# Kernel optimization log

Hardware: AMD Instinct MI355X
Metric: run time of the kernel (lower is better)

Reference implementation:

```python
import jax, jax.numpy as jnp
import numpy as np

# TT factorization of a 4096 -> 4096 linear layer
IN_SHAPE = (8, 8, 8, 8)    # input_tt_shape, prod = 4096
OUT_SHAPE = (8, 8, 8, 8)   # output_tt_shape, prod = 4096
RANKS = (1, 16, 16, 16, 1) # tt_ranks, len = n_dim + 1
N_DIM = len(IN_SHAPE)
BATCH = 2048
OUT_SIZE = int(np.prod(OUT_SHAPE))
IN_SIZE = int(np.prod(IN_SHAPE))


def setup_inputs() -> dict:
    key = jax.random.key(0)
    ks = jax.random.split(key, N_DIM + 1)
    x = jax.random.normal(ks[0], (BATCH, IN_SIZE), dtype=jnp.float32)
    inp = {"x": x}
    for i in range(N_DIM):
        rows = RANKS[i] * OUT_SHAPE[i]
        cols = IN_SHAPE[i] * RANKS[i + 1]
        # xavier_uniform scale, matching torch init statistics
        limit = float(np.sqrt(6.0 / (rows + cols)))
        inp[f"core{i}"] = jax.random.uniform(
            ks[i + 1], (rows, cols), minval=-limit, maxval=limit, dtype=jnp.float32
        )
    inp["bias"] = jnp.zeros((OUT_SIZE,), dtype=jnp.float32)
    return inp


def reference(x, core0, core1, core2, core3, bias):
    cores = [core0, core1, core2, core3]
    res = x  # [B, prod(IN_SHAPE)]
    # Sequential TT-core contraction, last mode first (faithful to torch loop)
    for k in range(N_DIM - 1, -1, -1):
        res = res.reshape(-1, IN_SHAPE[k])                     # [.., n_k]
        res = res.T                                            # [n_k, ..]
        res = res.reshape(RANKS[k + 1] * IN_SHAPE[k], -1)      # [r_{k+1}*n_k, ..]
        res = cores[k] @ res                                   # [r_k*m_k, ..]
    res = res.reshape(OUT_SIZE, -1).T                          # [B, prod(OUT_SHAPE)]
    return res + bias
```

## Files before the change

kernel.cpp:

```cpp
#include <hip/hip_runtime.h>
#include <hip/hip_bf16.h>
#include <stdint.h>


typedef __bf16 bf16_t;
typedef __bf16 bf16x8 __attribute__((ext_vector_type(8)));
typedef float floatx4 __attribute__((ext_vector_type(4)));

#define BATCH_N 2048
#define KD 4096
#define ND 4096

__device__ static inline void load_lds16(const void* g, void* l) {
    __builtin_amdgcn_global_load_lds(
        (const __attribute__((address_space(1))) void*)g,
        (__attribute__((address_space(3))) void*)l, 16, 0, 0);
}

__global__ __launch_bounds__(256) void cvt_x(const float* __restrict__ x,
                                             bf16_t* __restrict__ xb) {
    int t = blockIdx.x * 256 + threadIdx.x;
    const float4* xv = (const float4*)x;
    float4 a = xv[t * 2];
    float4 b = xv[t * 2 + 1];
    bf16x8 o;
    o[0] = (bf16_t)a.x; o[1] = (bf16_t)a.y; o[2] = (bf16_t)a.z; o[3] = (bf16_t)a.w;
    o[4] = (bf16_t)b.x; o[5] = (bf16_t)b.y; o[6] = (bf16_t)b.z; o[7] = (bf16_t)b.w;
    ((bf16x8*)xb)[t] = o;
}

__global__ __launch_bounds__(256) void build_w(const float* __restrict__ c0,
                                               const float* __restrict__ c1,
                                               const float* __restrict__ c2,
                                               const float* __restrict__ c3,
                                               bf16_t* __restrict__ W) {
    __shared__ float c0s[8 * 16];
    __shared__ float c1s[16 * 8 * 16];
    __shared__ float c2s[16 * 8 * 16];
    __shared__ float c3s[16 * 8];
    __shared__ float Ps[64 * 16];
    __shared__ float T1s[16 * 64];
    const int b = blockIdx.x;
    const int M23 = b >> 6, N01 = b & 63;
    const int n0 = N01 >> 3, n1 = N01 & 7, m2 = M23 >> 3, m3 = M23 & 7;
    const int t = threadIdx.x;

    if (t < 128) c0s[t] = c0[(t >> 4) * 128 + n0 * 16 + (t & 15)];
    if (t < 128) c3s[t] = c3[((t >> 3) * 8 + m3) * 8 + (t & 7)];
    for (int i = t; i < 2048; i += 256) {
        int r1 = i >> 7, m1 = (i >> 4) & 7, r2 = i & 15;
        c1s[i] = c1[(r1 * 8 + m1) * 128 + n1 * 16 + r2];
    }
    for (int i = t; i < 2048; i += 256) {
        int r2 = i >> 7, n2 = (i >> 4) & 7, r3 = i & 15;
        c2s[i] = c2[(r2 * 8 + m2) * 128 + n2 * 16 + r3];
    }
    __syncthreads();

    for (int i = t; i < 1024; i += 256) {
        int m01 = i >> 4, r2 = i & 15, m0 = m01 >> 3, m1 = m01 & 7;
        float s = 0.f;
#pragma unroll
        for (int r1 = 0; r1 < 16; ++r1)
            s += c0s[m0 * 16 + r1] * c1s[r1 * 128 + m1 * 16 + r2];
        Ps[i] = s;
    }
    for (int i = t; i < 1024; i += 256) {
        int r2 = i >> 6, n23 = i & 63, n2 = n23 >> 3, n3 = n23 & 7;
        float s = 0.f;
#pragma unroll
        for (int r3 = 0; r3 < 16; ++r3)
            s += c2s[r2 * 128 + n2 * 16 + r3] * c3s[r3 * 8 + n3];
        T1s[i] = s;
    }
    __syncthreads();

    const int n23 = t & 63, q = t >> 6;
#pragma unroll
    for (int g = 0; g < 16; ++g) {
        int m01 = q * 16 + g;
        float s = 0.f;
#pragma unroll
        for (int r2 = 0; r2 < 16; ++r2) s += Ps[m01 * 16 + r2] * T1s[r2 * 64 + n23];
        W[(size_t)(m01 * 64 + M23) * 4096 + N01 * 64 + n23] = (bf16_t)s;
    }
}

__global__ __launch_bounds__(256, 2) void gemm_bt(const bf16_t* __restrict__ A,
                                                  const bf16_t* __restrict__ B,
                                                  const float* __restrict__ bias,
                                                  float* __restrict__ C) {
    __shared__ bf16_t As[128 * 64];
    __shared__ bf16_t Bs[128 * 64];
    const int t = threadIdx.x;
    const int bn = blockIdx.x, bm = blockIdx.y;
    const int lane = t & 63, wave = t >> 6;
    const int wm = wave >> 1, wn = wave & 1;

    const int srow = lane >> 3;
    const int lc = (lane & 7) ^ srow;
    const bf16_t* Agp = A + (size_t)(bm * 128 + wave * 8 + srow) * KD + lc * 8;
    const bf16_t* Bgp = B + (size_t)(bn * 128 + wave * 8 + srow) * KD + lc * 8;
    bf16_t* AsW = As + wave * 512;
    bf16_t* BsW = Bs + wave * 512;

    floatx4 acc[4][4];
    floatx4 zero = {0.f, 0.f, 0.f, 0.f};
#pragma unroll
    for (int i = 0; i < 4; ++i)
#pragma unroll
        for (int j = 0; j < 4; ++j) acc[i][j] = zero;

    const int fr = lane & 15;
    const int fc = lane >> 4;

    for (int k0 = 0; k0 < KD; k0 += 64) {
        __syncthreads();
#pragma unroll
        for (int j = 0; j < 4; ++j) {
            load_lds16(Agp + (size_t)(j * 32) * KD + k0, AsW + j * 2048);
            load_lds16(Bgp + (size_t)(j * 32) * KD + k0, BsW + j * 2048);
        }
        __syncthreads();

#pragma unroll
        for (int kk = 0; kk < 2; ++kk) {
            const int pA = (fc + kk * 4) ^ (fr & 7);
            bf16x8 af[4], bf[4];
#pragma unroll
            for (int im = 0; im < 4; ++im)
                af[im] = *(const bf16x8*)(As + (wm * 64 + im * 16 + fr) * 64 + pA * 8);
#pragma unroll
            for (int in = 0; in < 4; ++in)
                bf[in] = *(const bf16x8*)(Bs + (wn * 64 + in * 16 + fr) * 64 + pA * 8);
#pragma unroll
            for (int im = 0; im < 4; ++im)
#pragma unroll
                for (int in = 0; in < 4; ++in)
                    acc[im][in] = __builtin_amdgcn_mfma_f32_16x16x32_bf16(
                        af[im], bf[in], acc[im][in], 0, 0, 0);
        }
    }

    const int rl = lane >> 4, cl = lane & 15;
    const size_t rbase = (size_t)bm * 128 + wm * 64;
    const int cbase = bn * 128 + wn * 64;
#pragma unroll
    for (int im = 0; im < 4; ++im) {
#pragma unroll
        for (int in = 0; in < 4; ++in) {
            int col = cbase + in * 16 + cl;
            float bv = bias[col];
#pragma unroll
            for (int r = 0; r < 4; ++r) {
                size_t row = rbase + im * 16 + rl * 4 + r;
                C[row * ND + col] = acc[im][in][r] + bv;
            }
        }
    }
}

extern "C" void kernel_launch(void* const* d_in, const int* in_sizes, int n_in,
                              void* d_out, int out_size, void* d_ws, size_t ws_size,
                              hipStream_t stream) {
    const float* x  = (const float*)d_in[0];
    const float* c0 = (const float*)d_in[1];
    const float* c1 = (const float*)d_in[2];
    const float* c2 = (const float*)d_in[3];
    const float* c3 = (const float*)d_in[4];
    const float* bias = (const float*)d_in[5];
    float* out = (float*)d_out;

    char* ws = (char*)d_ws;
    bf16_t* Xb = (bf16_t*)ws;
    bf16_t* W  = (bf16_t*)(ws + (16u << 20));

    cvt_x<<<4096, 256, 0, stream>>>(x, Xb);
    build_w<<<4096, 256, 0, stream>>>(c0, c1, c2, c3, W);
    dim3 grid(ND / 128, BATCH_N / 128);
    gemm_bt<<<grid, 256, 0, stream>>>(Xb, W, bias, out);
}
```

Measured before the change: 183.2 us.

## Replace LDS-tiled GEMM with register-direct loads and fuse prep kernels

The GEMM drops shared-memory staging and barriers. Each of two waves loads its A and B MFMA fragments straight from global memory into registers, double-buffered in 32-wide k steps, and each wave computes a 64x128 tile. The x conversion and W construction are merged into one launch to remove a kernel launch. The register path avoids LDS traffic and syncs but issues uncoalesced 16-byte row-strided global loads, gets no cross-wave reuse through LDS, and uses far more registers with fewer waves per block.

```diff
diff --git a/kernel.cpp b/kernel.cpp
--- a/kernel.cpp
+++ b/kernel.cpp
@@ -11,39 +11,36 @@
 #define KD 4096
 #define ND 4096
 
-__device__ static inline void load_lds16(const void* g, void* l) {
-    __builtin_amdgcn_global_load_lds(
-        (const __attribute__((address_space(1))) void*)g,
-        (__attribute__((address_space(3))) void*)l, 16, 0, 0);
-}
-
-__global__ __launch_bounds__(256) void cvt_x(const float* __restrict__ x,
-                                             bf16_t* __restrict__ xb) {
-    int t = blockIdx.x * 256 + threadIdx.x;
-    const float4* xv = (const float4*)x;
-    float4 a = xv[t * 2];
-    float4 b = xv[t * 2 + 1];
-    bf16x8 o;
-    o[0] = (bf16_t)a.x; o[1] = (bf16_t)a.y; o[2] = (bf16_t)a.z; o[3] = (bf16_t)a.w;
-    o[4] = (bf16_t)b.x; o[5] = (bf16_t)b.y; o[6] = (bf16_t)b.z; o[7] = (bf16_t)b.w;
-    ((bf16x8*)xb)[t] = o;
-}
-
-__global__ __launch_bounds__(256) void build_w(const float* __restrict__ c0,
-                                               const float* __restrict__ c1,
-                                               const float* __restrict__ c2,
-                                               const float* __restrict__ c3,
-                                               bf16_t* __restrict__ W) {
+__global__ __launch_bounds__(256) void prep(const float* __restrict__ x,
+                                            const float* __restrict__ c0,
+                                            const float* __restrict__ c1,
+                                            const float* __restrict__ c2,
+                                            const float* __restrict__ c3,
+                                            bf16_t* __restrict__ W,
+                                            bf16_t* __restrict__ xb) {
     __shared__ float c0s[8 * 16];
     __shared__ float c1s[16 * 8 * 16];
     __shared__ float c2s[16 * 8 * 16];
     __shared__ float c3s[16 * 8];
     __shared__ float Ps[64 * 16];
     __shared__ float T1s[16 * 64];
+    const int t = threadIdx.x;
+
+    if (blockIdx.x >= 4096) {
+        int g = (blockIdx.x - 4096) * 256 + t;
+        const float4* xv = (const float4*)x;
+        float4 a = xv[g * 2];
+        float4 b = xv[g * 2 + 1];
+        bf16x8 o;
+        o[0] = (bf16_t)a.x; o[1] = (bf16_t)a.y; o[2] = (bf16_t)a.z; o[3] = (bf16_t)a.w;
+        o[4] = (bf16_t)b.x; o[5] = (bf16_t)b.y; o[6] = (bf16_t)b.z; o[7] = (bf16_t)b.w;
+        ((bf16x8*)xb)[g] = o;
+        return;
+    }
+
     const int b = blockIdx.x;
     const int M23 = b >> 6, N01 = b & 63;
     const int n0 = N01 >> 3, n1 = N01 & 7, m2 = M23 >> 3, m3 = M23 & 7;
-    const int t = threadIdx.x;
 
     if (t < 128) c0s[t] = c0[(t >> 4) * 128 + n0 * 16 + (t & 15)];
     if (t < 128) c3s[t] = c3[((t >> 3) * 8 + m3) * 8 + (t & 7)];
@@ -86,69 +83,64 @@
     }
 }
 
-__global__ __launch_bounds__(256, 2) void gemm_bt(const bf16_t* __restrict__ A,
-                                                  const bf16_t* __restrict__ B,
-                                                  const float* __restrict__ bias,
-                                                  float* __restrict__ C) {
-    __shared__ bf16_t As[128 * 64];
-    __shared__ bf16_t Bs[128 * 64];
+__global__ __launch_bounds__(128, 2) void gemm_reg(const bf16_t* __restrict__ A,
+                                                   const bf16_t* __restrict__ B,
+                                                   const float* __restrict__ bias,
+                                                   float* __restrict__ C) {
     const int t = threadIdx.x;
+    const int lane = t & 63, wave = t >> 6;
     const int bn = blockIdx.x, bm = blockIdx.y;
-    const int lane = t & 63, wave = t >> 6;
-    const int wm = wave >> 1, wn = wave & 1;
+    const int fr = lane & 15;
+    const int fk = (lane >> 4) * 8;
 
-    const int srow = lane >> 3;
-    const int lc = (lane & 7) ^ srow;
-    const bf16_t* Agp = A + (size_t)(bm * 128 + wave * 8 + srow) * KD + lc * 8;
-    const bf16_t* Bgp = B + (size_t)(bn * 128 + wave * 8 + srow) * KD + lc * 8;
-    bf16_t* AsW = As + wave * 512;
-    bf16_t* BsW = Bs + wave * 512;
+    const bf16_t* Ap = A + (size_t)(bm * 128 + wave * 64 + fr) * KD + fk;
+    const bf16_t* Bp = B + (size_t)(bn * 128 + fr) * KD + fk;
 
-    floatx4 acc[4][4];
+    floatx4 acc[4][8];
     floatx4 zero = {0.f, 0.f, 0.f, 0.f};
 #pragma unroll
     for (int i = 0; i < 4; ++i)
 #pragma unroll
-        for (int j = 0; j < 4; ++j) acc[i][j] = zero;
+        for (int j = 0; j < 8; ++j) acc[i][j] = zero;
 
-    const int fr = lane & 15;
-    const int fc = lane >> 4;
+    bf16x8 a0[4], b0[8], a1[4], b1[8];
 
-    for (int k0 = 0; k0 < KD; k0 += 64) {
-        __syncthreads();
-#pragma unroll
-        for (int j = 0; j < 4; ++j) {
-            load_lds16(Agp + (size_t)(j * 32) * KD + k0, AsW + j * 2048);
-            load_lds16(Bgp + (size_t)(j * 32) * KD + k0, BsW + j * 2048);
-        }
-        __syncthreads();
-
-#pragma unroll
-        for (int kk = 0; kk < 2; ++kk) {
-            const int pA = (fc + kk * 4) ^ (fr & 7);
-            bf16x8 af[4], bf[4];
-#pragma unroll
-            for (int im = 0; im < 4; ++im)
-                af[im] = *(const bf16x8*)(As + (wm * 64 + im * 16 + fr) * 64 + pA * 8);
-#pragma unroll
-            for (int in = 0; in < 4; ++in)
-                bf[in] = *(const bf16x8*)(Bs + (wn * 64 + in * 16 + fr) * 64 + pA * 8);
-#pragma unroll
-            for (int im = 0; im < 4; ++im)
-#pragma unroll
-                for (int in = 0; in < 4; ++in)
-                    acc[im][in] = __builtin_amdgcn_mfma_f32_16x16x32_bf16(
-                        af[im], bf[in], acc[im][in], 0, 0, 0);
-        }
+#define LDA(f, k)                                                         \
+    {                                                                     \
+        _Pragma("unroll") for (int im = 0; im < 4; ++im)                  \
+            f[im] = *(const bf16x8*)(Ap + (size_t)(im * 16) * KD + (k));  \
+    }
+#define LDB(f, k)                                                         \
+    {                                                                     \
+        _Pragma("unroll") for (int in = 0; in < 8; ++in)                  \
+            f[in] = *(const bf16x8*)(Bp + (size_t)(in * 16) * KD + (k));  \
+    }
+#define MM(fa, fb)                                                        \
+    {                                                                     \
+        _Pragma("unroll") for (int im = 0; im < 4; ++im)                  \
+            _Pragma("unroll") for (int in = 0; in < 8; ++in)              \
+                acc[im][in] = __builtin_amdgcn_mfma_f32_16x16x32_bf16(    \
+                    fa[im], fb[in], acc[im][in], 0, 0, 0);                \
     }
 
+    LDA(a0, 0); LDB(b0, 0);
+    for (int kb = 0; kb < KD - 64; kb += 64) {
+        LDA(a1, kb + 32); LDB(b1, kb + 32);
+        MM(a0, b0);
+        LDA(a0, kb + 64); LDB(b0, kb + 64);
+        MM(a1, b1);
+    }
+    LDA(a1, KD - 32); LDB(b1, KD - 32);
+    MM(a0, b0);
+    MM(a1, b1);
+
     const int rl = lane >> 4, cl = lane & 15;
-    const size_t rbase = (size_t)bm * 128 + wm * 64;
-    const int cbase = bn * 128 + wn * 64;
+    const size_t rbase = (size_t)bm * 128 + wave * 64;
+    const int cbase = bn * 128;
 #pragma unroll
     for (int im = 0; im < 4; ++im) {
 #pragma unroll
-        for (int in = 0; in < 4; ++in) {
+        for (int in = 0; in < 8; ++in) {
             int col = cbase + in * 16 + cl;
             float bv = bias[col];
 #pragma unroll
@@ -158,6 +150,9 @@
             }
         }
     }
+#undef LDA
+#undef LDB
+#undef MM
 }
 
 extern "C" void kernel_launch(void* const* d_in, const int* in_sizes, int n_in,
@@ -175,8 +170,7 @@
     bf16_t* Xb = (bf16_t*)ws;
     bf16_t* W  = (bf16_t*)(ws + (16u << 20));
 
-    cvt_x<<<4096, 256, 0, stream>>>(x, Xb);
-    build_w<<<4096, 256, 0, stream>>>(c0, c1, c2, c3, W);
+    prep<<<8192, 256, 0, stream>>>(x, c0, c1, c2, c3, W, Xb);
     dim3 grid(ND / 128, BATCH_N / 128);
-    gemm_bt<<<grid, 256, 0, stream>>>(Xb, W, bias, out);
+    gemm_reg<<<grid, 128, 0, stream>>>(Xb, W, bias, out);
 }
```

Measured after the change: 307.7 us. +67.9%, slower.

## Pre-pack operands into MFMA fragment layout and load GEMM directly from global

Applied to the files above, without the earlier changes.

The X conversion and W construction kernels now write bf16 data already arranged in per-wave 16x32 MFMA fragment order. This lets the GEMM load operands straight into registers with double-buffered register prefetch, removing the LDS staging and both block barriers per k-step. build_w is also restructured so each block handles 16 output-row groups (256 blocks instead of 4096), reusing the loaded cores and writing vectorized fragments. In exchange, operands have no LDS reuse across waves, so each wave fetches its fragments from global/L2 independently, and the larger T1s array raises LDS use in build_w.

```diff
diff --git a/kernel.cpp b/kernel.cpp
--- a/kernel.cpp
+++ b/kernel.cpp
@@ -11,49 +11,48 @@
 #define KD 4096
 #define ND 4096
 
-__device__ static inline void load_lds16(const void* g, void* l) {
-    __builtin_amdgcn_global_load_lds(
-        (const __attribute__((address_space(1))) void*)g,
-        (__attribute__((address_space(3))) void*)l, 16, 0, 0);
-}
-
-__global__ __launch_bounds__(256) void cvt_x(const float* __restrict__ x,
-                                             bf16_t* __restrict__ xb) {
-    int t = blockIdx.x * 256 + threadIdx.x;
-    const float4* xv = (const float4*)x;
-    float4 a = xv[t * 2];
-    float4 b = xv[t * 2 + 1];
+__global__ __launch_bounds__(256) void cvt_x_frag(const float* __restrict__ x,
+                                                  bf16_t* __restrict__ Af) {
+    const int t = threadIdx.x;
+    const int fid = blockIdx.x * 4 + (t >> 6);
+    const int lane = t & 63;
+    const int mg = fid >> 7, kc = fid & 127;
+    const int row = mg * 16 + (lane & 15);
+    const int k = kc * 32 + (lane >> 4) * 8;
+    const float4* xp = (const float4*)(x + (size_t)row * KD + k);
+    float4 a = xp[0], b = xp[1];
     bf16x8 o;
     o[0] = (bf16_t)a.x; o[1] = (bf16_t)a.y; o[2] = (bf16_t)a.z; o[3] = (bf16_t)a.w;
     o[4] = (bf16_t)b.x; o[5] = (bf16_t)b.y; o[6] = (bf16_t)b.z; o[7] = (bf16_t)b.w;
-    ((bf16x8*)xb)[t] = o;
+    ((bf16x8*)(Af + (size_t)fid * 512))[lane] = o;
 }
 
 __global__ __launch_bounds__(256) void build_w(const float* __restrict__ c0,
                                                const float* __restrict__ c1,
                                                const float* __restrict__ c2,
                                                const float* __restrict__ c3,
-                                               bf16_t* __restrict__ W) {
-    __shared__ float c0s[8 * 16];
-    __shared__ float c1s[16 * 8 * 16];
-    __shared__ float c2s[16 * 8 * 16];
-    __shared__ float c3s[16 * 8];
+                                               bf16_t* __restrict__ Bf) {
+    __shared__ float c0s[128];
+    __shared__ float c1s[2048];
+    __shared__ float c2s[2 * 2048];
+    __shared__ float c3s[1024];
     __shared__ float Ps[64 * 16];
-    __shared__ float T1s[16 * 64];
+    __shared__ float T1s[16 * 1025];
     const int b = blockIdx.x;
-    const int M23 = b >> 6, N01 = b & 63;
-    const int n0 = N01 >> 3, n1 = N01 & 7, m2 = M23 >> 3, m3 = M23 & 7;
+    const int M23b = b >> 6, N01 = b & 63;
+    const int n0 = N01 >> 3, n1 = N01 & 7;
     const int t = threadIdx.x;
 
     if (t < 128) c0s[t] = c0[(t >> 4) * 128 + n0 * 16 + (t & 15)];
-    if (t < 128) c3s[t] = c3[((t >> 3) * 8 + m3) * 8 + (t & 7)];
+    for (int i = t; i < 1024; i += 256) c3s[i] = c3[i];
     for (int i = t; i < 2048; i += 256) {
         int r1 = i >> 7, m1 = (i >> 4) & 7, r2 = i & 15;
         c1s[i] = c1[(r1 * 8 + m1) * 128 + n1 * 16 + r2];
     }
-    for (int i = t; i < 2048; i += 256) {
-        int r2 = i >> 7, n2 = (i >> 4) & 7, r3 = i & 15;
-        c2s[i] = c2[(r2 * 8 + m2) * 128 + n2 * 16 + r3];
+    for (int i = t; i < 4096; i += 256) {
+        int m2l = i >> 11, j = i & 2047;
+        int r2 = j >> 7, n2 = (j >> 4) & 7, r3 = j & 15;
+        c2s[i] = c2[(r2 * 8 + M23b * 2 + m2l) * 128 + n2 * 16 + r3];
     }
     __syncthreads();
 
@@ -65,44 +64,51 @@
             s += c0s[m0 * 16 + r1] * c1s[r1 * 128 + m1 * 16 + r2];
         Ps[i] = s;
     }
-    for (int i = t; i < 1024; i += 256) {
-        int r2 = i >> 6, n23 = i & 63, n2 = n23 >> 3, n3 = n23 & 7;
+    for (int i = t; i < 16384; i += 256) {
+        int m23l = i >> 10, r2 = (i >> 6) & 15, n23 = i & 63;
+        int m2l = m23l >> 3, m3 = m23l & 7, n2 = n23 >> 3, n3 = n23 & 7;
         float s = 0.f;
 #pragma unroll
         for (int r3 = 0; r3 < 16; ++r3)
-            s += c2s[r2 * 128 + n2 * 16 + r3] * c3s[r3 * 8 + n3];
-        T1s[i] = s;
+            s += c2s[m2l * 2048 + r2 * 128 + n2 * 16 + r3] * c3s[r3 * 64 + m3 * 8 + n3];
+        T1s[m23l * 1025 + r2 * 64 + n23] = s;
     }
     __syncthreads();
 
-    const int n23 = t & 63, q = t >> 6;
+    const int m23l = t & 15, lhi = (t >> 4) & 3, q = t >> 6;
+    const int lane = t & 63;
 #pragma unroll
-    for (int g = 0; g < 16; ++g) {
-        int m01 = q * 16 + g;
-        float s = 0.f;
+    for (int mi = 0; mi < 16; ++mi) {
+        int m01 = q * 16 + mi;
 #pragma unroll
-        for (int r2 = 0; r2 < 16; ++r2) s += Ps[m01 * 16 + r2] * T1s[r2 * 64 + n23];
-        W[(size_t)(m01 * 64 + M23) * 4096 + N01 * 64 + n23] = (bf16_t)s;
+        for (int n23h = 0; n23h < 2; ++n23h) {
+            int n23b = n23h * 32 + lhi * 8;
+            bf16x8 o;
+#pragma unroll
+            for (int n3l = 0; n3l < 8; ++n3l) {
+                float s = 0.f;
+#pragma unroll
+                for (int r2 = 0; r2 < 16; ++r2)
+                    s += Ps[m01 * 16 + r2] * T1s[m23l * 1025 + r2 * 64 + n23b + n3l];
+                o[n3l] = (bf16_t)s;
+            }
+            size_t ng = m01 * 4 + M23b, kc = N01 * 2 + n23h;
+            ((bf16x8*)(Bf + (ng * 128 + kc) * 512))[lane] = o;
+        }
     }
 }
 
-__global__ __launch_bounds__(256, 2) void gemm_bt(const bf16_t* __restrict__ A,
-                                                  const bf16_t* __restrict__ B,
-                                                  const float* __restrict__ bias,
-                                                  float* __restrict__ C) {
-    __shared__ bf16_t As[128 * 64];
-    __shared__ bf16_t Bs[128 * 64];
+__global__ __launch_bounds__(256) void gemm_frag(const bf16_t* __restrict__ Af,
+                                                 const bf16_t* __restrict__ Bf,
+                                                 const float* __restrict__ bias,
+                                                 float* __restrict__ C) {
     const int t = threadIdx.x;
-    const int bn = blockIdx.x, bm = blockIdx.y;
     const int lane = t & 63, wave = t >> 6;
     const int wm = wave >> 1, wn = wave & 1;
+    const int bn = blockIdx.x, bm = blockIdx.y;
 
-    const int srow = lane >> 3;
-    const int lc = (lane & 7) ^ srow;
-    const bf16_t* Agp = A + (size_t)(bm * 128 + wave * 8 + srow) * KD + lc * 8;
-    const bf16_t* Bgp = B + (size_t)(bn * 128 + wave * 8 + srow) * KD + lc * 8;
-    bf16_t* AsW = As + wave * 512;
-    bf16_t* BsW = Bs + wave * 512;
+    const bf16_t* Ap = Af + (size_t)(bm * 8 + wm * 4) * 65536 + (size_t)lane * 8;
+    const bf16_t* Bp = Bf + (size_t)(bn * 8 + wn * 4) * 65536 + (size_t)lane * 8;
 
     floatx4 acc[4][4];
     floatx4 zero = {0.f, 0.f, 0.f, 0.f};
@@ -111,36 +117,35 @@
 #pragma unroll
         for (int j = 0; j < 4; ++j) acc[i][j] = zero;
 
-    const int fr = lane & 15;
-    const int fc = lane >> 4;
+    bf16x8 av[2][4], bv[2][4];
 
-    for (int k0 = 0; k0 < KD; k0 += 64) {
-        __syncthreads();
-#pragma unroll
-        for (int j = 0; j < 4; ++j) {
-            load_lds16(Agp + (size_t)(j * 32) * KD + k0, AsW + j * 2048);
-            load_lds16(Bgp + (size_t)(j * 32) * KD + k0, BsW + j * 2048);
-        }
-        __syncthreads();
+#define LD(buf, kc)                                                           \
+    {                                                                         \
+        _Pragma("unroll") for (int im = 0; im < 4; ++im)                      \
+            av[buf][im] = *(const bf16x8*)(Ap + (size_t)im * 65536 + (kc) * 512); \
+        _Pragma("unroll") for (int in = 0; in < 4; ++in)                      \
+            bv[buf][in] = *(const bf16x8*)(Bp + (size_t)in * 65536 + (kc) * 512); \
+    }
+#define MM(buf)                                                               \
+    {                                                                         \
+        _Pragma("unroll") for (int im = 0; im < 4; ++im)                      \
+            _Pragma("unroll") for (int in = 0; in < 4; ++in)                  \
+                acc[im][in] = __builtin_amdgcn_mfma_f32_16x16x32_bf16(        \
+                    av[buf][im], bv[buf][in], acc[im][in], 0, 0, 0);          \
+    }
 
-#pragma unroll
-        for (int kk = 0; kk < 2; ++kk) {
-            const int pA = (fc + kk * 4) ^ (fr & 7);
-            bf16x8 af[4], bf[4];
-#pragma unroll
-            for (int im = 0; im < 4; ++im)
-                af[im] = *(const bf16x8*)(As + (wm * 64 + im * 16 + fr) * 64 + pA * 8);
-#pragma unroll
-            for (int in = 0; in < 4; ++in)
-                bf[in] = *(const bf16x8*)(Bs + (wn * 64 + in * 16 + fr) * 64 + pA * 8);
-#pragma unroll
-            for (int im = 0; im < 4; ++im)
-#pragma unroll
-                for (int in = 0; in < 4; ++in)
-                    acc[im][in] = __builtin_amdgcn_mfma_f32_16x16x32_bf16(
-                        af[im], bf[in], acc[im][in], 0, 0, 0);
-        }
+    LD(0, 0);
+    LD(1, 1);
+    for (int kc = 0; kc < 124; kc += 2) {
+        MM(0); LD(0, kc + 2);
+        MM(1); LD(1, kc + 3);
     }
+    MM(0); LD(0, 126);
+    MM(1); LD(1, 127);
+    MM(0);
+    MM(1);
+#undef LD
+#undef MM
 
     const int rl = lane >> 4, cl = lane & 15;
     const size_t rbase = (size_t)bm * 128 + wm * 64;
@@ -150,11 +155,11 @@
 #pragma unroll
         for (int in = 0; in < 4; ++in) {
             int col = cbase + in * 16 + cl;
-            float bv = bias[col];
+            float bv2 = bias[col];
 #pragma unroll
             for (int r = 0; r < 4; ++r) {
                 size_t row = rbase + im * 16 + rl * 4 + r;
-                C[row * ND + col] = acc[im][in][r] + bv;
+                C[row * ND + col] = acc[im][in][r] + bv2;
             }
         }
     }
@@ -175,8 +180,8 @@
     bf16_t* Xb = (bf16_t*)ws;
     bf16_t* W  = (bf16_t*)(ws + (16u << 20));
 
-    cvt_x<<<4096, 256, 0, stream>>>(x, Xb);
-    build_w<<<4096, 256, 0, stream>>>(c0, c1, c2, c3, W);
+    cvt_x_frag<<<4096, 256, 0, stream>>>(x, Xb);
+    build_w<<<256, 256, 0, stream>>>(c0, c1, c2, c3, W);
     dim3 grid(ND / 128, BATCH_N / 128);
-    gemm_bt<<<grid, 256, 0, stream>>>(Xb, W, bias, out);
+    gemm_frag<<<grid, 256, 0, stream>>>(Xb, W, bias, out);
 }
```

New measurement: 212.3 us. +15.9%, slower.

## Split-K GEMM with atomic accumulation, merge prep kernels, bias-init output

Applied to the files above, without the earlier changes.

Merges the x conversion and W construction into one prep launch with blocks dispatched by index. Splits the GEMM K dimension in two across blockIdx.z, which doubles the grid from 512 to 1024 blocks, and raises launch bounds to 4 waves per SIMD. Partial results are combined with float atomicAdd into an output that a new init_out kernel pre-fills with bias. The aim is better CU occupancy and fewer launches, at the cost of an extra 32MB output write pass, atomic traffic, and nondeterministic summation order.

```diff
diff --git a/kernel.cpp b/kernel.cpp
--- a/kernel.cpp
+++ b/kernel.cpp
@@ -17,33 +17,36 @@
         (__attribute__((address_space(3))) void*)l, 16, 0, 0);
 }
 
-__global__ __launch_bounds__(256) void cvt_x(const float* __restrict__ x,
-                                             bf16_t* __restrict__ xb) {
-    int t = blockIdx.x * 256 + threadIdx.x;
-    const float4* xv = (const float4*)x;
-    float4 a = xv[t * 2];
-    float4 b = xv[t * 2 + 1];
-    bf16x8 o;
-    o[0] = (bf16_t)a.x; o[1] = (bf16_t)a.y; o[2] = (bf16_t)a.z; o[3] = (bf16_t)a.w;
-    o[4] = (bf16_t)b.x; o[5] = (bf16_t)b.y; o[6] = (bf16_t)b.z; o[7] = (bf16_t)b.w;
-    ((bf16x8*)xb)[t] = o;
-}
-
-__global__ __launch_bounds__(256) void build_w(const float* __restrict__ c0,
-                                               const float* __restrict__ c1,
-                                               const float* __restrict__ c2,
-                                               const float* __restrict__ c3,
-                                               bf16_t* __restrict__ W) {
+__global__ __launch_bounds__(256) void prep(const float* __restrict__ x,
+                                            const float* __restrict__ c0,
+                                            const float* __restrict__ c1,
+                                            const float* __restrict__ c2,
+                                            const float* __restrict__ c3,
+                                            bf16_t* __restrict__ W,
+                                            bf16_t* __restrict__ xb) {
     __shared__ float c0s[8 * 16];
     __shared__ float c1s[16 * 8 * 16];
     __shared__ float c2s[16 * 8 * 16];
     __shared__ float c3s[16 * 8];
     __shared__ float Ps[64 * 16];
     __shared__ float T1s[16 * 64];
+    const int t = threadIdx.x;
+
+    if (blockIdx.x >= 4096) {
+        int g = (blockIdx.x - 4096) * 256 + t;
+        const float4* xv = (const float4*)x;
+        float4 a = xv[g * 2];
+        float4 b = xv[g * 2 + 1];
+        bf16x8 o;
+        o[0] = (bf16_t)a.x; o[1] = (bf16_t)a.y; o[2] = (bf16_t)a.z; o[3] = (bf16_t)a.w;
+        o[4] = (bf16_t)b.x; o[5] = (bf16_t)b.y; o[6] = (bf16_t)b.z; o[7] = (bf16_t)b.w;
+        ((bf16x8*)xb)[g] = o;
+        return;
+    }
+
     const int b = blockIdx.x;
     const int M23 = b >> 6, N01 = b & 63;
     const int n0 = N01 >> 3, n1 = N01 & 7, m2 = M23 >> 3, m3 = M23 & 7;
-    const int t = threadIdx.x;
 
     if (t < 128) c0s[t] = c0[(t >> 4) * 128 + n0 * 16 + (t & 15)];
     if (t < 128) c3s[t] = c3[((t >> 3) * 8 + m3) * 8 + (t & 7)];
@@ -86,14 +89,21 @@
     }
 }
 
-__global__ __launch_bounds__(256, 2) void gemm_bt(const bf16_t* __restrict__ A,
+__global__ __launch_bounds__(256) void init_out(const float* __restrict__ bias,
+                                                float* __restrict__ C) {
+    int idx = blockIdx.x * 256 + threadIdx.x;
+    int col = (idx * 4) & (ND - 1);
+    float4 bv = *(const float4*)(bias + col);
+    ((float4*)C)[idx] = bv;
+}
+
+__global__ __launch_bounds__(256, 4) void gemm_bt(const bf16_t* __restrict__ A,
                                                   const bf16_t* __restrict__ B,
-                                                  const float* __restrict__ bias,
                                                   float* __restrict__ C) {
     __shared__ bf16_t As[128 * 64];
     __shared__ bf16_t Bs[128 * 64];
     const int t = threadIdx.x;
-    const int bn = blockIdx.x, bm = blockIdx.y;
+    const int bn = blockIdx.x, bm = blockIdx.y, kz = blockIdx.z;
     const int lane = t & 63, wave = t >> 6;
     const int wm = wave >> 1, wn = wave & 1;
 
@@ -114,7 +124,8 @@
     const int fr = lane & 15;
     const int fc = lane >> 4;
 
-    for (int k0 = 0; k0 < KD; k0 += 64) {
+    const int kbeg = kz * (KD / 2);
+    for (int k0 = kbeg; k0 < kbeg + KD / 2; k0 += 64) {
         __syncthreads();
 #pragma unroll
         for (int j = 0; j < 4; ++j) {
@@ -150,11 +161,10 @@
 #pragma unroll
         for (int in = 0; in < 4; ++in) {
             int col = cbase + in * 16 + cl;
-            float bv = bias[col];
 #pragma unroll
             for (int r = 0; r < 4; ++r) {
                 size_t row = rbase + im * 16 + rl * 4 + r;
-                C[row * ND + col] = acc[im][in][r] + bv;
+                atomicAdd(&C[row * ND + col], acc[im][in][r]);
             }
         }
     }
@@ -175,8 +185,8 @@
     bf16_t* Xb = (bf16_t*)ws;
     bf16_t* W  = (bf16_t*)(ws + (16u << 20));
 
-    cvt_x<<<4096, 256, 0, stream>>>(x, Xb);
-    build_w<<<4096, 256, 0, stream>>>(c0, c1, c2, c3, W);
-    dim3 grid(ND / 128, BATCH_N / 128);
-    gemm_bt<<<grid, 256, 0, stream>>>(Xb, W, bias, out);
+    prep<<<8192, 256, 0, stream>>>(x, c0, c1, c2, c3, W, Xb);
+    init_out<<<8192, 256, 0, stream>>>(bias, out);
+    dim3 grid(ND / 128, BATCH_N / 128, 2);
+    gemm_bt<<<grid, 256, 0, stream>>>(Xb, W, out);
 }
```

Result: slower. 221.5 us (+20.9%).
